# Kernel tuning notes

Hardware: AMD Instinct MI355X
Metric: run time of the kernel (lower is better)

The kernel has to match this reference:

```python
import jax, jax.numpy as jnp
import numpy as np

N_NODES = 50000
N_EDGES = 800000
ATOM_DIM = 32
EDGE_DIM = 16
HIDDEN = 64
NUM_STEPS = 3
NUM_GRAPHS = 256
OUT_DIM = 1


def setup_inputs() -> dict:
    key = jax.random.key(0)
    ks = jax.random.split(key, 20)
    s = 0.05
    inp = {
        "x": jax.random.normal(ks[0], (N_NODES, ATOM_DIM), dtype=jnp.float32),
        "edge_index": jax.random.randint(ks[1], (2, N_EDGES), 0, N_NODES),
        "edge_attr": jax.random.normal(ks[2], (N_EDGES, EDGE_DIM), dtype=jnp.float32),
        "batch": jnp.sort(jax.random.randint(ks[3], (N_NODES,), 0, NUM_GRAPHS)),
        # atom embedding
        "W_embed": jax.random.normal(ks[4], (ATOM_DIM, HIDDEN)) * s,
        "b_embed": jnp.zeros((HIDDEN,)),
        # message MLP: Linear(2H+E, H) -> ReLU -> Linear(H, H)
        "W_m1": jax.random.normal(ks[5], (2 * HIDDEN + EDGE_DIM, HIDDEN)) * s,
        "b_m1": jnp.zeros((HIDDEN,)),
        "W_m2": jax.random.normal(ks[6], (HIDDEN, HIDDEN)) * s,
        "b_m2": jnp.zeros((HIDDEN,)),
        # GRUCell (torch layout: [3H, in] stacked r,z,n)
        "W_ih": jax.random.normal(ks[7], (3 * HIDDEN, HIDDEN)) * s,
        "b_ih": jnp.zeros((3 * HIDDEN,)),
        "W_hh": jax.random.normal(ks[8], (3 * HIDDEN, HIDDEN)) * s,
        "b_hh": jnp.zeros((3 * HIDDEN,)),
        # head: Linear(2H, H) -> ReLU -> Linear(H, out)
        "W_h1": jax.random.normal(ks[9], (2 * HIDDEN, HIDDEN)) * s,
        "b_h1": jnp.zeros((HIDDEN,)),
        "W_h2": jax.random.normal(ks[10], (HIDDEN, OUT_DIM)) * s,
        "b_h2": jnp.zeros((OUT_DIM,)),
    }
    return inp


def _gru_cell(inp, h, W_ih, b_ih, W_hh, b_hh):
    gi = inp @ W_ih.T + b_ih   # [N, 3H]
    gh = h @ W_hh.T + b_hh     # [N, 3H]
    i_r, i_z, i_n = jnp.split(gi, 3, axis=-1)
    h_r, h_z, h_n = jnp.split(gh, 3, axis=-1)
    r = jax.nn.sigmoid(i_r + h_r)
    z = jax.nn.sigmoid(i_z + h_z)
    n = jnp.tanh(i_n + r * h_n)
    return (1.0 - z) * n + z * h


def reference(x, edge_index, edge_attr, batch,
              W_embed, b_embed, W_m1, b_m1, W_m2, b_m2,
              W_ih, b_ih, W_hh, b_hh, W_h1, b_h1, W_h2, b_h2):
    h = x @ W_embed + b_embed                       # [N, H]
    src, dst = edge_index[0], edge_index[1]         # PyG: x_j = x[src], x_i = x[dst]
    for _ in range(NUM_STEPS):                      # tied weights
        m = jnp.concatenate([h[src], h[dst], edge_attr], axis=-1)  # [E, 2H+ED]
        m = jax.nn.relu(m @ W_m1 + b_m1) @ W_m2 + b_m2             # [E, H]
        agg = jax.ops.segment_sum(m, dst, num_segments=N_NODES)    # scatter-add
        h = _gru_cell(agg, h, W_ih, b_ih, W_hh, b_hh)
    g_sum = jax.ops.segment_sum(h, batch, num_segments=NUM_GRAPHS)  # [G, H]
    cnt = jax.ops.segment_sum(jnp.ones((N_NODES,), h.dtype), batch,
                              num_segments=NUM_GRAPHS)
    g_mean = g_sum / jnp.maximum(cnt, 1.0)[:, None]
    g = jnp.concatenate([g_sum, g_mean], axis=-1)   # [G, 2H]
    return jax.nn.relu(g @ W_h1 + b_h1) @ W_h2 + b_h2  # [G, out]
```

## Files before the change

kernel.cpp:

```cpp
#include <hip/hip_runtime.h>
#include <math.h>

#define NN 50000
#define NE 800000
#define AD 32
#define ED 16
#define HD 64
#define NG 256
#define NTILES (NE / 16)
#define EGRID 1280
#define TPX (NTILES / 8)
#define GGRID 768
#define GTILES (NN / 16)
#define PGRID 782

typedef short bf16x8 __attribute__((ext_vector_type(8)));
typedef float f32x4  __attribute__((ext_vector_type(4)));
union U4B { uint4 u; bf16x8 v; };

__device__ __forceinline__ float blo(unsigned u){ return __uint_as_float(u << 16); }
__device__ __forceinline__ float bhi(unsigned u){ return __uint_as_float(u & 0xffff0000u); }
__device__ __forceinline__ unsigned short f2bf(float f){
  unsigned u = __float_as_uint(f);
  u += 0x7fffu + ((u >> 16) & 1u);
  return (unsigned short)(u >> 16);
}
__device__ __forceinline__ unsigned packbf2(float a, float b){
  return (unsigned)f2bf(a) | ((unsigned)f2bf(b) << 16);
}
__device__ __forceinline__ bf16x8 ldfrag_g(const unsigned* p){
  U4B x; x.u = *(const uint4*)p; return x.v;
}
__device__ __forceinline__ unsigned srp1(unsigned a, unsigned b, unsigned c){
  float lo = fmaxf(blo(a) + blo(b) + blo(c), 0.f);
  float hi = fmaxf(bhi(a) + bhi(b) + bhi(c), 0.f);
  return packbf2(lo, hi);
}
__device__ __forceinline__ bf16x8 srp4(uint4 a, uint4 b, uint4 c){
  U4B r;
  r.u.x = srp1(a.x, b.x, c.x);
  r.u.y = srp1(a.y, b.y, c.y);
  r.u.z = srp1(a.z, b.z, c.z);
  r.u.w = srp1(a.w, b.w, c.w);
  return r.v;
}

__global__ __launch_bounds__(256) void k_prep(const float* __restrict__ W1,
                                              const float* __restrict__ W2,
                                              const float* __restrict__ Wih,
                                              const float* __restrict__ Whh,
                                              const float* __restrict__ b1,
                                              unsigned short* __restrict__ W1Tp,
                                              unsigned short* __restrict__ W2Tp,
                                              unsigned short* __restrict__ Wgru,
                                              unsigned short* __restrict__ W1cTp)
{
  int idx = blockIdx.x * 256 + threadIdx.x;
  if (idx < 64 * 168){
    int n = idx / 168, k = idx % 168;
    W1Tp[idx] = (k < 144) ? f2bf(W1[k * 64 + n]) : (unsigned short)0;
    return;
  }
  idx -= 64 * 168;
  if (idx < 64 * 72){
    int n = idx / 72, k = idx % 72;
    W2Tp[idx] = (k < 64) ? f2bf(W2[k * 64 + n]) : (unsigned short)0;
    return;
  }
  idx -= 64 * 72;
  if (idx < 384 * 64){
    int j = idx & 7;
    int g = (idx >> 3) % 384;
    int blk = idx >> 3; blk /= 384;
    int q = blk & 3, ks = blk >> 2;
    int k = ks * 32 + q * 8 + j;
    float v = (g < 192) ? Wih[g * 64 + k] : Whh[(g - 192) * 64 + k];
    Wgru[idx] = f2bf(v);
    return;
  }
  idx -= 384 * 64;
  if (idx < 64 * 32){
    int n = idx / 32, k = idx % 32;
    float v = (k < 16) ? W1[(128 + k) * 64 + n] : (k == 16 ? b1[n] : 0.f);
    W1cTp[idx] = f2bf(v);
  }
}

__global__ __launch_bounds__(256) void k_hist(const int* __restrict__ eidx, int* __restrict__ deg)
{
  int e = blockIdx.x * 256 + threadIdx.x;
  if (e < NE) atomicAdd(&deg[eidx[NE + e]], 1);
}

__global__ __launch_bounds__(1024) void k_scan1(const int* __restrict__ deg,
                                                int* __restrict__ cur,
                                                int* __restrict__ bsum)
{
  __shared__ int s[1024];
  const int t = threadIdx.x;
  const int idx = blockIdx.x * 1024 + t;
  int v = (idx < NN) ? deg[idx] : 0;
  s[t] = v;
  __syncthreads();
  for (int d = 1; d < 1024; d <<= 1){
    int y = (t >= d) ? s[t - d] : 0;
    __syncthreads();
    s[t] += y;
    __syncthreads();
  }
  if (idx < NN) cur[idx] = s[t] - v;
  if (t == 1023) bsum[blockIdx.x] = s[1023];
}

__global__ __launch_bounds__(64) void k_scan2(const int* __restrict__ bsum,
                                              int* __restrict__ bpre)
{
  const int t = threadIdx.x;
  const int nb = (NN + 1023) / 1024;
  int v = (t < nb) ? bsum[t] : 0;
  int orig = v;
  #pragma unroll
  for (int off = 1; off < 64; off <<= 1){
    int u = __shfl_up(v, off);
    if (t >= off) v += u;
  }
  if (t < nb) bpre[t] = v - orig;
}

__global__ __launch_bounds__(1024) void k_scan3(int* __restrict__ cur,
                                                const int* __restrict__ bpre)
{
  const int idx = blockIdx.x * 1024 + threadIdx.x;
  if (idx < NN) cur[idx] += bpre[blockIdx.x];
}

__global__ __launch_bounds__(256) void k_scatter(const int* __restrict__ eidx,
                                                 int* __restrict__ cur,
                                                 int4* __restrict__ sde)
{
  int e = blockIdx.x * 256 + threadIdx.x;
  if (e >= NE) return;
  int s = eidx[e];
  int d = eidx[NE + e];
  int p = atomicAdd(&cur[d], 1);
  sde[p] = make_int4(s, d, e, 0);
}

__global__ __launch_bounds__(256) void k_eprep(const float* __restrict__ eattr,
                                               const unsigned* __restrict__ W1cTp32,
                                               unsigned* __restrict__ E1o)
{
  const int t = threadIdx.x, lane = t & 63, wv = t >> 6;
  const int m = lane & 15, q = lane >> 4;
  bf16x8 wf[4];
  #pragma unroll
  for (int tl = 0; tl < 4; ++tl)
    wf[tl] = ldfrag_g(W1cTp32 + (tl * 16 + m) * 16 + q * 4);

  for (int wt = blockIdx.x * 4 + wv; wt < NTILES; wt += 1024 * 4){
    const int base = wt * 16;
    U4B x;
    if (q < 2){
      const float* ea = eattr + (size_t)(base + m) * 16 + q * 8;
      float4 v0 = *(const float4*)(ea);
      float4 v1 = *(const float4*)(ea + 4);
      x.u.x = packbf2(v0.x, v0.y); x.u.y = packbf2(v0.z, v0.w);
      x.u.z = packbf2(v1.x, v1.y); x.u.w = packbf2(v1.z, v1.w);
    } else if (q == 2) x.u = make_uint4(0x3F80u, 0, 0, 0);
    else               x.u = make_uint4(0, 0, 0, 0);
    bf16x8 a = x.v;
    f32x4 c[4];
    #pragma unroll
    for (int tl = 0; tl < 4; ++tl) c[tl] = f32x4{0.f,0.f,0.f,0.f};
    #pragma unroll
    for (int tl = 0; tl < 4; ++tl)
      c[tl] = __builtin_amdgcn_mfma_f32_16x16x32_bf16(a, wf[tl], c[tl], 0, 0, 0);
    #pragma unroll
    for (int tl = 0; tl < 4; ++tl){
      #pragma unroll
      for (int rr = 0; rr < 4; ++rr){
        float v = c[tl][rr];
        float pp = __shfl_xor(v, 1);
        if (!(m & 1))
          E1o[(size_t)(base + q * 4 + rr) * 32 + (tl * 16 + m) / 2] = packbf2(v, pp);
      }
    }
  }
}

__global__ __launch_bounds__(256, 4) void k_pre(const unsigned* __restrict__ h_bf,
                                                const unsigned short* __restrict__ W1Tp,
                                                unsigned* __restrict__ C12)
{
  const int t = threadIdx.x, lane = t & 63, wv = t >> 6;
  const int m = lane & 15, q = lane >> 4;
  bf16x8 wa[4][2], wb[4][2];
  #pragma unroll
  for (int tl = 0; tl < 4; ++tl)
    #pragma unroll
    for (int ks = 0; ks < 2; ++ks){
      wa[tl][ks] = ldfrag_g((const unsigned*)(W1Tp + (tl * 16 + m) * 168 + ks * 32 + q * 8));
      wb[tl][ks] = ldfrag_g((const unsigned*)(W1Tp + (tl * 16 + m) * 168 + 64 + ks * 32 + q * 8));
    }
  for (int wt = blockIdx.x * 4 + wv; wt < GTILES; wt += PGRID * 4){
    const int n0 = wt * 16;
    bf16x8 aH[2];
    #pragma unroll
    for (int ks = 0; ks < 2; ++ks)
      aH[ks] = ldfrag_g(h_bf + (size_t)(n0 + m) * 32 + ks * 16 + q * 4);
    f32x4 ca[4], cb[4];
    #pragma unroll
    for (int tl = 0; tl < 4; ++tl){ ca[tl] = f32x4{0.f,0.f,0.f,0.f}; cb[tl] = ca[tl]; }
    #pragma unroll
    for (int ks = 0; ks < 2; ++ks)
      #pragma unroll
      for (int tl = 0; tl < 4; ++tl){
        ca[tl] = __builtin_amdgcn_mfma_f32_16x16x32_bf16(aH[ks], wa[tl][ks], ca[tl], 0, 0, 0);
        cb[tl] = __builtin_amdgcn_mfma_f32_16x16x32_bf16(aH[ks], wb[tl][ks], cb[tl], 0, 0, 0);
      }
    #pragma unroll
    for (int tl = 0; tl < 4; ++tl){
      #pragma unroll
      for (int rr = 0; rr < 4; ++rr){
        const int node = n0 + q * 4 + rr;
        float va = ca[tl][rr], vb = cb[tl][rr];
        float pa = __shfl_xor(va, 1), pb = __shfl_xor(vb, 1);
        if (!(m & 1)){
          C12[(size_t)node * 64 + (tl * 16 + m) / 2]      = packbf2(va, pa);
          C12[(size_t)node * 64 + 32 + (tl * 16 + m) / 2] = packbf2(vb, pb);
        }
      }
    }
  }
}

__global__ __launch_bounds__(256) void k_embed(const float* __restrict__ x,
                                               const float* __restrict__ We,
                                               const float* __restrict__ be,
                                               float* __restrict__ h,
                                               unsigned* __restrict__ h_bf,
                                               float* __restrict__ agg)
{
  const int t = threadIdx.x;
  const int j = t & 63, nd = t >> 6;
  const int node = blockIdx.x * 4 + nd;
  const float* xr = x + (size_t)node * AD;
  float acc = be[j];
  #pragma unroll 8
  for (int k = 0; k < AD; ++k)
    acc += xr[k] * We[k * HD + j];
  h[(size_t)node * HD + j] = acc;
  agg[(size_t)node * HD + j] = 0.f;
  float p = __shfl_down(acc, 1);
  if (!(j & 1)) h_bf[(size_t)node * 32 + (j >> 1)] = packbf2(acc, p);
}

__global__ __launch_bounds__(256, 4) void k_edge(const unsigned* __restrict__ C12,
                                                 const unsigned* __restrict__ E1o,
                                                 const int4* __restrict__ sde,
                                                 const unsigned* __restrict__ W2Tp32,
                                                 const float* __restrict__ b2,
                                                 float* __restrict__ agg)
{
  const int t = threadIdx.x;
  const int lane = t & 63, wv = t >> 6;
  const int m = lane & 15, q = lane >> 4;

  bf16x8 w2f[4][2];
  #pragma unroll
  for (int tl = 0; tl < 4; ++tl)
    #pragma unroll
    for (int ks = 0; ks < 2; ++ks)
      w2f[tl][ks] = ldfrag_g(W2Tp32 + (tl * 16 + m) * 36 + ks * 16 + q * 4);

  float b2v[4];
  #pragma unroll
  for (int tl = 0; tl < 4; ++tl) b2v[tl] = b2[tl * 16 + m];

  const int xcd = blockIdx.x & 7, bi = blockIdx.x >> 3;
  const int wend = (xcd + 1) * TPX;
  const int wstep = (EGRID / 8) * 4;
  int wt = xcd * TPX + bi * 4 + wv;

  int4 cursde = sde[wt * 16 + m];

  while (wt < wend){
    const int wn = wt + wstep;
    const bool hasn = (wn < wend);
    int4 nsde = make_int4(0, 0, 0, 0);
    if (hasn) nsde = sde[wn * 16 + m];

    const int scur = cursde.x, dcur = cursde.y, ecur = cursde.z;

    const unsigned* c1p = C12 + (size_t)scur * 64;
    const unsigned* c2p = C12 + (size_t)dcur * 64 + 32;
    const unsigned* e1p = E1o + (size_t)ecur * 32;
    uint4 c1a = *(const uint4*)(c1p + q * 4);
    uint4 c1b = *(const uint4*)(c1p + 16 + q * 4);
    uint4 c2a = *(const uint4*)(c2p + q * 4);
    uint4 c2b = *(const uint4*)(c2p + 16 + q * 4);
    uint4 e1a = *(const uint4*)(e1p + q * 4);
    uint4 e1b = *(const uint4*)(e1p + 16 + q * 4);

    bf16x8 af0 = srp4(c1a, c2a, e1a);
    bf16x8 af1 = srp4(c1b, c2b, e1b);

    f32x4 o0 = {0.f,0.f,0.f,0.f}, o1 = o0, o2 = o0, o3 = o0;
    o0 = __builtin_amdgcn_mfma_f32_16x16x32_bf16(af0, w2f[0][0], o0, 0, 0, 0);
    o1 = __builtin_amdgcn_mfma_f32_16x16x32_bf16(af0, w2f[1][0], o1, 0, 0, 0);
    o2 = __builtin_amdgcn_mfma_f32_16x16x32_bf16(af0, w2f[2][0], o2, 0, 0, 0);
    o3 = __builtin_amdgcn_mfma_f32_16x16x32_bf16(af0, w2f[3][0], o3, 0, 0, 0);
    o0 = __builtin_amdgcn_mfma_f32_16x16x32_bf16(af1, w2f[0][1], o0, 0, 0, 0);
    o1 = __builtin_amdgcn_mfma_f32_16x16x32_bf16(af1, w2f[1][1], o1, 0, 0, 0);
    o2 = __builtin_amdgcn_mfma_f32_16x16x32_bf16(af1, w2f[2][1], o2, 0, 0, 0);
    o3 = __builtin_amdgcn_mfma_f32_16x16x32_bf16(af1, w2f[3][1], o3, 0, 0, 0);

    int prev = __shfl_up(dcur, 1);
    bool isStart = (m == 0) || (dcur != prev);
    unsigned long long bal = __ballot(isStart);
    unsigned bs = (unsigned)bal & 0xFFFFu;
    int nr = __popc(bs);
    unsigned rem = bs & (bs - 1);
    int lo = 0;
    for (int r = 0; r < nr; ++r){
      int hi = rem ? (__ffs(rem) - 1) : 16;
      rem &= rem - 1;
      float s0 = 0.f, s1 = 0.f, s2 = 0.f, s3 = 0.f;
      #pragma unroll
      for (int rr = 0; rr < 4; ++rr){
        int row = q * 4 + rr;
        bool in = (row >= lo) && (row < hi);
        s0 += in ? o0[rr] : 0.f;
        s1 += in ? o1[rr] : 0.f;
        s2 += in ? o2[rr] : 0.f;
        s3 += in ? o3[rr] : 0.f;
      }
      s0 += __shfl_xor(s0, 16); s0 += __shfl_xor(s0, 32);
      s1 += __shfl_xor(s1, 16); s1 += __shfl_xor(s1, 32);
      s2 += __shfl_xor(s2, 16); s2 += __shfl_xor(s2, 32);
      s3 += __shfl_xor(s3, 16); s3 += __shfl_xor(s3, 32);
      int d = __shfl(dcur, lo);
      float cntf = (float)(hi - lo);
      if (q == 0){
        float v0 = s0 + cntf * b2v[0];
        float v1 = s1 + cntf * b2v[1];
        float v2 = s2 + cntf * b2v[2];
        float v3 = s3 + cntf * b2v[3];
        float* dp = &agg[(size_t)d * HD + m];
        if (r == 0 || r == nr - 1){
          atomicAdd(dp +  0, v0); atomicAdd(dp + 16, v1);
          atomicAdd(dp + 32, v2); atomicAdd(dp + 48, v3);
        } else {
          dp[ 0] = v0; dp[16] = v1; dp[32] = v2; dp[48] = v3;
        }
      }
      lo = hi;
    }

    wt = wn; cursde = nsde;
  }
}

__global__ __launch_bounds__(256) void k_gru(float* __restrict__ agg,
                                             float* __restrict__ h,
                                             unsigned* __restrict__ h_bf,
                                             const unsigned short* __restrict__ Wgru,
                                             const float* __restrict__ bih,
                                             const float* __restrict__ bhh)
{
  __shared__ __align__(16) unsigned short sWg[384 * 64];

  const int t = threadIdx.x;
  {
    const uint4* srcp = (const uint4*)Wgru;
    uint4* dstp = (uint4*)sWg;
    for (int i = t; i < 384 * 64 * 2 / 16; i += 256) dstp[i] = srcp[i];
  }
  __syncthreads();

  const int lane = t & 63, wv = t >> 6;
  const int m = lane & 15, q = lane >> 4;

  float bi_r[4], bi_z[4], bi_n[4], bh_r[4], bh_z[4], bh_n[4];
  #pragma unroll
  for (int tl = 0; tl < 4; ++tl){
    bi_r[tl] = bih[tl * 16 + m];  bi_z[tl] = bih[64 + tl * 16 + m];  bi_n[tl] = bih[128 + tl * 16 + m];
    bh_r[tl] = bhh[tl * 16 + m];  bh_z[tl] = bhh[64 + tl * 16 + m];  bh_n[tl] = bhh[128 + tl * 16 + m];
  }

  for (int wt = blockIdx.x * 4 + wv; wt < GTILES; wt += GGRID * 4){
    const int n0 = wt * 16;

    bf16x8 aA[2], aH[2];
    #pragma unroll
    for (int ks = 0; ks < 2; ++ks){
      const float* ap = agg + (size_t)(n0 + m) * 64 + ks * 32 + q * 8;
      float4 v0 = *(const float4*)ap;
      float4 v1 = *(const float4*)(ap + 4);
      U4B x;
      x.u.x = packbf2(v0.x, v0.y); x.u.y = packbf2(v0.z, v0.w);
      x.u.z = packbf2(v1.x, v1.y); x.u.w = packbf2(v1.z, v1.w);
      aA[ks] = x.v;
      aH[ks] = ldfrag_g(h_bf + (size_t)(n0 + m) * 32 + ks * 16 + q * 4);
    }

    f32x4 ci[12], ch[12];
    #pragma unroll
    for (int tl = 0; tl < 12; ++tl){ ci[tl] = f32x4{0.f,0.f,0.f,0.f}; ch[tl] = ci[tl]; }
    #pragma unroll
    for (int ks = 0; ks < 2; ++ks){
      #pragma unroll
      for (int tl = 0; tl < 12; ++tl){
        bf16x8 bi = *(const bf16x8*)&sWg[((ks * 4 + q) * 384 + tl * 16 + m) * 8];
        ci[tl] = __builtin_amdgcn_mfma_f32_16x16x32_bf16(aA[ks], bi, ci[tl], 0, 0, 0);
        bf16x8 bh = *(const bf16x8*)&sWg[((ks * 4 + q) * 384 + 192 + tl * 16 + m) * 8];
        ch[tl] = __builtin_amdgcn_mfma_f32_16x16x32_bf16(aH[ks], bh, ch[tl], 0, 0, 0);
      }
    }

    #pragma unroll
    for (int tl = 0; tl < 4; ++tl){
      #pragma unroll
      for (int rr = 0; rr < 4; ++rr){
        const int node = n0 + q * 4 + rr;
        float ir = ci[tl][rr]     + bi_r[tl], hr = ch[tl][rr]     + bh_r[tl];
        float iz = ci[4 + tl][rr] + bi_z[tl], hz = ch[4 + tl][rr] + bh_z[tl];
        float in_ = ci[8 + tl][rr] + bi_n[tl], hn = ch[8 + tl][rr] + bh_n[tl];
        float rg = 1.f / (1.f + __expf(-(ir + hr)));
        float zg = 1.f / (1.f + __expf(-(iz + hz)));
        float ng = tanhf(in_ + rg * hn);
        float hold = h[(size_t)node * HD + tl * 16 + m];
        float hnew = (1.f - zg) * ng + zg * hold;
        h[(size_t)node * HD + tl * 16 + m] = hnew;
        agg[(size_t)node * HD + tl * 16 + m] = 0.f;
        float pp = __shfl_xor(hnew, 1);
        if (!(m & 1))
          h_bf[(size_t)node * 32 + tl * 8 + (m >> 1)] = packbf2(hnew, pp);
      }
    }
  }
}

__global__ __launch_bounds__(256) void k_pool(const float* __restrict__ h,
                                              const int* __restrict__ batch,
                                              float* __restrict__ gsum,
                                              float* __restrict__ cnt)
{
  const int t = threadIdx.x;
  const int j = t & 63, r = t >> 6;
  const int n0 = blockIdx.x * 64 + r * 16;
  float acc = 0.f, c = 0.f;
  int cur = -1;
  for (int i = 0; i < 16; ++i){
    int n = n0 + i;
    if (n >= NN) break;
    int g = batch[n];
    if (g != cur){
      if (cur >= 0){
        atomicAdd(&gsum[cur * HD + j], acc);
        if (j == 0) atomicAdd(&cnt[cur], c);
      }
      cur = g; acc = 0.f; c = 0.f;
    }
    acc += h[(size_t)n * HD + j];
    c += 1.f;
  }
  if (cur >= 0){
    atomicAdd(&gsum[cur * HD + j], acc);
    if (j == 0) atomicAdd(&cnt[cur], c);
  }
}

__global__ __launch_bounds__(64) void k_head(const float* __restrict__ gsum,
                                             const float* __restrict__ cnt,
                                             const float* __restrict__ W1,
                                             const float* __restrict__ b1,
                                             const float* __restrict__ W2,
                                             const float* __restrict__ b2,
                                             float* __restrict__ out)
{
  __shared__ float gv[128];
  const int g = blockIdx.x, j = threadIdx.x;
  float s = gsum[g * HD + j];
  float c = cnt[g];
  gv[j] = s;
  gv[64 + j] = s / fmaxf(c, 1.f);
  __syncthreads();
  float acc = b1[j];
  #pragma unroll 8
  for (int k = 0; k < 128; ++k)
    acc += gv[k] * W1[k * HD + j];
  acc = fmaxf(acc, 0.f);
  float v = acc * W2[j];
  #pragma unroll
  for (int off = 32; off; off >>= 1) v += __shfl_down(v, off, 64);
  if (j == 0) out[g] = v + b2[0];
}

extern "C" void kernel_launch(void* const* d_in, const int* in_sizes, int n_in,
                              void* d_out, int out_size, void* d_ws, size_t ws_size,
                              hipStream_t stream)
{
  (void)in_sizes; (void)n_in; (void)out_size; (void)ws_size;
  const float* x     = (const float*)d_in[0];
  const int*   eidx  = (const int*)d_in[1];
  const float* eattr = (const float*)d_in[2];
  const int*   batch = (const int*)d_in[3];
  const float* We    = (const float*)d_in[4];
  const float* be    = (const float*)d_in[5];
  const float* Wm1   = (const float*)d_in[6];
  const float* bm1   = (const float*)d_in[7];
  const float* Wm2   = (const float*)d_in[8];
  const float* bm2   = (const float*)d_in[9];
  const float* Wih   = (const float*)d_in[10];
  const float* bih   = (const float*)d_in[11];
  const float* Whh   = (const float*)d_in[12];
  const float* bhh   = (const float*)d_in[13];
  const float* Wh1   = (const float*)d_in[14];
  const float* bh1   = (const float*)d_in[15];
  const float* Wh2   = (const float*)d_in[16];
  const float* bh2   = (const float*)d_in[17];

  char* w = (char*)d_ws;
  float* h     = (float*)w;                      w += (size_t)NN * HD * 4;
  unsigned* h_bf = (unsigned*)w;                 w += (size_t)NN * 32 * 4;
  float* agg   = (float*)w;                      w += (size_t)NN * HD * 4;
  int*   deg   = (int*)w;                        w += (size_t)NN * 4;
  int*   cur   = (int*)w;                        w += (size_t)NN * 4;
  int4*  sde   = (int4*)w;                       w += (size_t)NE * 16;
  int*   bsum  = (int*)w;                        w += 64 * 4;
  int*   bpre  = (int*)w;                        w += 64 * 4;
  unsigned short* W1Tp = (unsigned short*)w;     w += 64 * 168 * 2;
  unsigned short* W2Tp = (unsigned short*)w;     w += 64 * 72 * 2;
  unsigned short* Wgru = (unsigned short*)w;     w += 384 * 64 * 2;
  unsigned short* W1cTp = (unsigned short*)w;    w += 64 * 32 * 2;
  float* gsum  = (float*)w;                      w += (size_t)NG * HD * 4;
  float* cnt   = (float*)w;                      w += (size_t)NG * 4;
  unsigned* C12 = (unsigned*)w;                  w += (size_t)NN * 64 * 4;
  unsigned* E1o = (unsigned*)w;                  w += (size_t)NE * 32 * 4;

  const int nscanb = (NN + 1023) / 1024;

  k_prep<<<164, 256, 0, stream>>>(Wm1, Wm2, Wih, Whh, bm1, W1Tp, W2Tp, Wgru, W1cTp);
  hipMemsetAsync(deg, 0, (size_t)NN * 4, stream);
  k_hist<<<(NE + 255) / 256, 256, 0, stream>>>(eidx, deg);
  k_scan1<<<nscanb, 1024, 0, stream>>>(deg, cur, bsum);
  k_scan2<<<1, 64, 0, stream>>>(bsum, bpre);
  k_scan3<<<nscanb, 1024, 0, stream>>>(cur, bpre);
  k_scatter<<<(NE + 255) / 256, 256, 0, stream>>>(eidx, cur, sde);
  k_eprep<<<1024, 256, 0, stream>>>(eattr, (const unsigned*)W1cTp, E1o);

  k_embed<<<NN / 4, 256, 0, stream>>>(x, We, be, h, h_bf, agg);
  for (int s = 0; s < 3; ++s){
    k_pre<<<PGRID, 256, 0, stream>>>(h_bf, W1Tp, C12);
    k_edge<<<EGRID, 256, 0, stream>>>(C12, E1o, sde, (const unsigned*)W2Tp, bm2, agg);
    k_gru<<<GGRID, 256, 0, stream>>>(agg, h, h_bf, Wgru, bih, bhh);
  }
  hipMemsetAsync(gsum, 0, (size_t)(NG * HD + NG) * 4, stream);
  k_pool<<<(NN + 63) / 64, 256, 0, stream>>>(h, batch, gsum, cnt);
  k_head<<<NG, 64, 0, stream>>>(gsum, cnt, Wh1, bh1, Wh2, bh2, (float*)d_out);
}
```

Before: 594.6 us.

## Store edge features in sorted order and partition hist/scatter atomics by XCD

```diff
diff --git a/kernel.cpp b/kernel.cpp
--- a/kernel.cpp
+++ b/kernel.cpp
@@ -13,6 +13,10 @@
 #define GGRID 768
 #define GTILES (NN / 16)
 #define PGRID 782
+#define SGRID 1024
+#define HGRID 1024
+#define EPGRID 1024
+#define NPX (NN / 8)
 
 typedef short bf16x8 __attribute__((ext_vector_type(8)));
 typedef float f32x4  __attribute__((ext_vector_type(4)));
@@ -88,8 +92,12 @@
 
 __global__ __launch_bounds__(256) void k_hist(const int* __restrict__ eidx, int* __restrict__ deg)
 {
-  int e = blockIdx.x * 256 + threadIdx.x;
-  if (e < NE) atomicAdd(&deg[eidx[NE + e]], 1);
+  const int g = blockIdx.x & 7, bi = blockIdx.x >> 3;
+  const int lo = g * NPX, hi = lo + NPX;
+  for (int e = bi * 256 + threadIdx.x; e < NE; e += (HGRID / 8) * 256){
+    int d = eidx[NE + e];
+    if (d >= lo && d < hi) atomicAdd(&deg[d], 1);
+  }
 }
 
 __global__ __launch_bounds__(1024) void k_scan1(const int* __restrict__ deg,
@@ -138,17 +146,23 @@
                                                  int* __restrict__ cur,
                                                  int4* __restrict__ sde)
 {
-  int e = blockIdx.x * 256 + threadIdx.x;
-  if (e >= NE) return;
-  int s = eidx[e];
-  int d = eidx[NE + e];
-  int p = atomicAdd(&cur[d], 1);
-  sde[p] = make_int4(s, d, e, 0);
-}
-
-__global__ __launch_bounds__(256) void k_eprep(const float* __restrict__ eattr,
+  const int g = blockIdx.x & 7, bi = blockIdx.x >> 3;
+  const int lo = g * NPX, hi = lo + NPX;
+  for (int e = bi * 256 + threadIdx.x; e < NE; e += (SGRID / 8) * 256){
+    int d = eidx[NE + e];
+    if (d >= lo && d < hi){
+      int s = eidx[e];
+      int p = atomicAdd(&cur[d], 1);
+      sde[p] = make_int4(s, d, e, 0);
+    }
+  }
+}
+
+__global__ __launch_bounds__(256) void k_eprep(const int4* __restrict__ sde,
+                                               const float* __restrict__ eattr,
                                                const unsigned* __restrict__ W1cTp32,
-                                               unsigned* __restrict__ E1o)
+                                               unsigned* __restrict__ E1s,
+                                               int2* __restrict__ sd8)
 {
   const int t = threadIdx.x, lane = t & 63, wv = t >> 6;
   const int m = lane & 15, q = lane >> 4;
@@ -157,11 +171,13 @@
   for (int tl = 0; tl < 4; ++tl)
     wf[tl] = ldfrag_g(W1cTp32 + (tl * 16 + m) * 16 + q * 4);
 
-  for (int wt = blockIdx.x * 4 + wv; wt < NTILES; wt += 1024 * 4){
+  for (int wt = blockIdx.x * 4 + wv; wt < NTILES; wt += EPGRID * 4){
     const int base = wt * 16;
+    int4 rec = sde[base + m];
+    if (q == 0) sd8[base + m] = make_int2(rec.x, rec.y);
     U4B x;
     if (q < 2){
-      const float* ea = eattr + (size_t)(base + m) * 16 + q * 8;
+      const float* ea = eattr + (size_t)rec.z * 16 + q * 8;
       float4 v0 = *(const float4*)(ea);
       float4 v1 = *(const float4*)(ea + 4);
       x.u.x = packbf2(v0.x, v0.y); x.u.y = packbf2(v0.z, v0.w);
@@ -182,7 +198,7 @@
         float v = c[tl][rr];
         float pp = __shfl_xor(v, 1);
         if (!(m & 1))
-          E1o[(size_t)(base + q * 4 + rr) * 32 + (tl * 16 + m) / 2] = packbf2(v, pp);
+          E1s[(size_t)(base + q * 4 + rr) * 32 + (tl * 16 + m) / 2] = packbf2(v, pp);
       }
     }
   }
@@ -256,8 +272,8 @@
 }
 
 __global__ __launch_bounds__(256, 4) void k_edge(const unsigned* __restrict__ C12,
-                                                 const unsigned* __restrict__ E1o,
-                                                 const int4* __restrict__ sde,
+                                                 const unsigned* __restrict__ E1s,
+                                                 const int2* __restrict__ sd8,
                                                  const unsigned* __restrict__ W2Tp32,
                                                  const float* __restrict__ b2,
                                                  float* __restrict__ agg)
@@ -282,19 +298,19 @@
   const int wstep = (EGRID / 8) * 4;
   int wt = xcd * TPX + bi * 4 + wv;
 
-  int4 cursde = sde[wt * 16 + m];
+  int2 cursd = sd8[wt * 16 + m];
 
   while (wt < wend){
     const int wn = wt + wstep;
     const bool hasn = (wn < wend);
-    int4 nsde = make_int4(0, 0, 0, 0);
-    if (hasn) nsde = sde[wn * 16 + m];
-
-    const int scur = cursde.x, dcur = cursde.y, ecur = cursde.z;
+    int2 nsd = make_int2(0, 0);
+    if (hasn) nsd = sd8[wn * 16 + m];
+
+    const int scur = cursd.x, dcur = cursd.y;
 
     const unsigned* c1p = C12 + (size_t)scur * 64;
     const unsigned* c2p = C12 + (size_t)dcur * 64 + 32;
-    const unsigned* e1p = E1o + (size_t)ecur * 32;
+    const unsigned* e1p = E1s + (size_t)(wt * 16 + m) * 32;
     uint4 c1a = *(const uint4*)(c1p + q * 4);
     uint4 c1b = *(const uint4*)(c1p + 16 + q * 4);
     uint4 c2a = *(const uint4*)(c2p + q * 4);
@@ -357,7 +373,7 @@
       lo = hi;
     }
 
-    wt = wn; cursde = nsde;
+    wt = wn; cursd = nsd;
   }
 }
 
@@ -528,32 +544,33 @@
   int*   deg   = (int*)w;                        w += (size_t)NN * 4;
   int*   cur   = (int*)w;                        w += (size_t)NN * 4;
   int4*  sde   = (int4*)w;                       w += (size_t)NE * 16;
+  int2*  sd8   = (int2*)w;                       w += (size_t)NE * 8;
   int*   bsum  = (int*)w;                        w += 64 * 4;
   int*   bpre  = (int*)w;                        w += 64 * 4;
   unsigned short* W1Tp = (unsigned short*)w;     w += 64 * 168 * 2;
   unsigned short* W2Tp = (unsigned short*)w;     w += 64 * 72 * 2;
   unsigned short* Wgru = (unsigned short*)w;     w += 384 * 64 * 2;
-  unsigned short* W1cTp = (unsigned short*)w;    w += 64 * 32 * 2;
+  unsigned short* W1cTp = (unsigned short*)w;    w += 64 * 32 * 2 + 192;
   float* gsum  = (float*)w;                      w += (size_t)NG * HD * 4;
   float* cnt   = (float*)w;                      w += (size_t)NG * 4;
   unsigned* C12 = (unsigned*)w;                  w += (size_t)NN * 64 * 4;
-  unsigned* E1o = (unsigned*)w;                  w += (size_t)NE * 32 * 4;
+  unsigned* E1s = (unsigned*)w;                  w += (size_t)NE * 32 * 4;
 
   const int nscanb = (NN + 1023) / 1024;
 
   k_prep<<<164, 256, 0, stream>>>(Wm1, Wm2, Wih, Whh, bm1, W1Tp, W2Tp, Wgru, W1cTp);
   hipMemsetAsync(deg, 0, (size_t)NN * 4, stream);
-  k_hist<<<(NE + 255) / 256, 256, 0, stream>>>(eidx, deg);
+  k_hist<<<HGRID, 256, 0, stream>>>(eidx, deg);
   k_scan1<<<nscanb, 1024, 0, stream>>>(deg, cur, bsum);
   k_scan2<<<1, 64, 0, stream>>>(bsum, bpre);
   k_scan3<<<nscanb, 1024, 0, stream>>>(cur, bpre);
-  k_scatter<<<(NE + 255) / 256, 256, 0, stream>>>(eidx, cur, sde);
-  k_eprep<<<1024, 256, 0, stream>>>(eattr, (const unsigned*)W1cTp, E1o);
+  k_scatter<<<SGRID, 256, 0, stream>>>(eidx, cur, sde);
+  k_eprep<<<EPGRID, 256, 0, stream>>>(sde, eattr, (const unsigned*)W1cTp, E1s, sd8);
 
   k_embed<<<NN / 4, 256, 0, stream>>>(x, We, be, h, h_bf, agg);
   for (int s = 0; s < 3; ++s){
     k_pre<<<PGRID, 256, 0, stream>>>(h_bf, W1Tp, C12);
-    k_edge<<<EGRID, 256, 0, stream>>>(C12, E1o, sde, (const unsigned*)W2Tp, bm2, agg);
+    k_edge<<<EGRID, 256, 0, stream>>>(C12, E1s, sd8, (const unsigned*)W2Tp, bm2, agg);
     k_gru<<<GGRID, 256, 0, stream>>>(agg, h, h_bf, Wgru, bih, bhh);
   }
   hipMemsetAsync(gsum, 0, (size_t)(NG * HD + NG) * 4, stream);
```

Result: no change. 600.3 us (+1.0%).
